# Optimization experiments

Measured on AMD Instinct MI355X. Metric: run time of the kernel, lower is better.

The kernel has to match this reference:

```python
import jax, jax.numpy as jnp
import numpy as np

N_EMBD = 1024
N_HEAD = 16
LATENT = 64
HEAD_DIM = N_EMBD // N_HEAD
B, T = 2, 2048
SCALE = 1.0 / np.sqrt(LATENT)


def setup_inputs() -> dict:
    key = jax.random.key(0)
    ks = jax.random.split(key, 10)
    s = lambda fan_in: 1.0 / np.sqrt(fan_in)
    return {
        "x": jax.random.normal(ks[0], (B, T, N_EMBD), dtype=jnp.float32),
        "Wq": jax.random.normal(ks[1], (N_EMBD, N_EMBD), dtype=jnp.float32) * s(N_EMBD),
        "bq": jnp.zeros((N_EMBD,), dtype=jnp.float32),
        "Wk": jax.random.normal(ks[2], (N_EMBD, N_HEAD * LATENT), dtype=jnp.float32) * s(N_EMBD),
        "bk": jnp.zeros((N_HEAD * LATENT,), dtype=jnp.float32),
        "Wv": jax.random.normal(ks[3], (N_EMBD, N_HEAD * LATENT), dtype=jnp.float32) * s(N_EMBD),
        "bv": jnp.zeros((N_HEAD * LATENT,), dtype=jnp.float32),
        "Wo": jax.random.normal(ks[4], (N_HEAD * LATENT, N_EMBD), dtype=jnp.float32) * s(N_HEAD * LATENT),
        "bo": jnp.zeros((N_EMBD,), dtype=jnp.float32),
        "Wc": jax.random.normal(ks[5], (HEAD_DIM, LATENT), dtype=jnp.float32) * s(HEAD_DIM),
    }


def reference(x, Wq, bq, Wk, bk, Wv, bv, Wo, bo, Wc):
    Bv, Tv, C = x.shape
    # projections
    q = (x @ Wq + bq).reshape(Bv, Tv, N_HEAD, HEAD_DIM)        # [B,T,H,Dh]
    k = (x @ Wk + bk).reshape(Bv, Tv, N_HEAD, LATENT)          # [B,T,H,L]
    v = (x @ Wv + bv).reshape(Bv, Tv, N_HEAD, LATENT)          # [B,T,H,L]
    # compress q into latent dim: [B,T,H,L]
    qc = jnp.einsum("bthd,dl->bthl", q, Wc)
    # attention scores [B,H,T,T]
    att = jnp.einsum("bthl,bshl->bhts", qc, k) * SCALE
    causal = jnp.tril(jnp.ones((Tv, Tv), dtype=bool))
    att = jnp.where(causal[None, None], att, -jnp.inf)
    att = jax.nn.softmax(att, axis=-1)
    y = jnp.einsum("bhts,bshl->bthl", att, v).reshape(Bv, Tv, N_HEAD * LATENT)
    return y @ Wo + bo
```

## Files before the change

### kernel.cpp

```cpp
#include <hip/hip_runtime.h>
#include <stdint.h>

#define TT 2048
#define BB 2
#define MROWS (BB*TT)
#define LSCALE 0.18033688011112043f

typedef unsigned short u16;
typedef __bf16 bf16x8 __attribute__((ext_vector_type(8)));
typedef float f32x4 __attribute__((ext_vector_type(4)));
typedef short s16x8 __attribute__((ext_vector_type(8)));
typedef unsigned short u16x4 __attribute__((ext_vector_type(4)));

#define GLOBAL_AS const __attribute__((address_space(1))) void*
#define LDS_AS __attribute__((address_space(3))) void*

__device__ __forceinline__ u16 f2b(float f){
  uint32_t u = __builtin_bit_cast(uint32_t, f);
  u = (u + 0x7FFFu + ((u >> 16) & 1u)) >> 16;
  return (u16)u;
}

__global__ void cvt_bf16(const float* __restrict__ in, u16* __restrict__ out, int n4){
  int i = blockIdx.x * 256 + threadIdx.x;
  if (i < n4){
    float4 v = ((const float4*)in)[i];
    u16x4 o; o.x = f2b(v.x); o.y = f2b(v.y); o.z = f2b(v.z); o.w = f2b(v.w);
    ((u16x4*)out)[i] = o;
  }
}

__global__ __launch_bounds__(256) void build_wqc(const float* __restrict__ Wq,
                                                 const float* __restrict__ Wc,
                                                 float* __restrict__ Wqc){
  __shared__ float wc[4096];
  const int t = threadIdx.x;
  #pragma unroll
  for (int i = 0; i < 16; ++i) wc[i * 256 + t] = Wc[i * 256 + t];
  __syncthreads();
  const int idx = blockIdx.x * 256 + t;
  const int d = idx >> 6;
  const int h = (idx >> 2) & 15;
  const int lq = idx & 3;
  float wqr[64];
  const float4* wq4 = (const float4*)(Wq + (size_t)d * 1024 + h * 64);
  #pragma unroll
  for (int i = 0; i < 16; ++i){
    float4 v = wq4[i];
    wqr[i * 4 + 0] = v.x; wqr[i * 4 + 1] = v.y; wqr[i * 4 + 2] = v.z; wqr[i * 4 + 3] = v.w;
  }
  float* outp = Wqc + (size_t)d * 1024 + h * 64 + lq * 16;
  #pragma unroll
  for (int j = 0; j < 16; ++j){
    int lc = lq * 16 + j;
    float acc = 0.f;
    #pragma unroll
    for (int dd = 0; dd < 64; ++dd) acc += wqr[dd] * wc[dd * 64 + lc];
    outp[j] = acc;
  }
}

__global__ void build_bqc(const float* __restrict__ bq, const float* __restrict__ Wc,
                          float* __restrict__ bqc){
  int n = blockIdx.x * 256 + threadIdx.x;
  int h = n >> 6, lc = n & 63;
  float acc = 0.f;
  for (int dd = 0; dd < 64; ++dd) acc += bq[h * 64 + dd] * Wc[dd * 64 + lc];
  bqc[n] = acc;
}

__global__ void transpose_w4(const float* __restrict__ s0, const float* __restrict__ s1,
                             const float* __restrict__ s2, const float* __restrict__ s3,
                             u16* __restrict__ o0, u16* __restrict__ o1,
                             u16* __restrict__ o2, u16* __restrict__ o3){
  const int z = blockIdx.z;
  const float* in = (z == 0) ? s0 : (z == 1) ? s1 : (z == 2) ? s2 : s3;
  u16* out = (z == 0) ? o0 : (z == 1) ? o1 : (z == 2) ? o2 : o3;
  __shared__ float t[32][33];
  int tx = threadIdx.x & 31, ty = threadIdx.x >> 5;
  int c0 = blockIdx.x * 32, r0 = blockIdx.y * 32;
  #pragma unroll
  for (int i = 0; i < 32; i += 8)
    t[ty + i][tx] = in[(size_t)(r0 + ty + i) * 1024 + c0 + tx];
  __syncthreads();
  #pragma unroll
  for (int i = 0; i < 32; i += 8)
    out[(size_t)(c0 + ty + i) * 1024 + r0 + tx] = f2b(t[tx][ty + i]);
}

__global__ void transpose_v(const u16* __restrict__ vb, u16* __restrict__ vt){
  __shared__ u16 t[32][34];
  int tx = threadIdx.x & 31, ty = threadIdx.x >> 5;
  int s0 = blockIdx.x * 32, d0 = blockIdx.y * 32, bh = blockIdx.z;
  int b = bh >> 4, h = bh & 15;
  #pragma unroll
  for (int i = 0; i < 32; i += 8)
    t[ty + i][tx] = vb[(size_t)(b * TT + s0 + ty + i) * 1024 + h * 64 + d0 + tx];
  __syncthreads();
  #pragma unroll
  for (int i = 0; i < 32; i += 8)
    vt[((size_t)bh * 64 + d0 + ty + i) * TT + s0 + tx] = t[tx][ty + i];
}

__device__ __forceinline__ void gemm_tile(const u16* __restrict__ A, const u16* __restrict__ BT,
                                          int m0, int n0, int K, f32x4 (&acc)[4][4],
                                          u16* As, u16* Bs, int tid){
  const int wv = tid >> 6, l = tid & 63;
  const int aoff = ((wv >> 1) * 64 + (l & 15)) * 32 + ((l >> 4) << 3);
  const int boff = ((wv & 1) * 64 + (l & 15)) * 32 + ((l >> 4) << 3);
  const int ob0 = wv * 1024 + l * 16;
  for (int kt = 0; kt < K; kt += 32){
    __syncthreads();
    #pragma unroll
    for (int j = 0; j < 2; ++j){
      int ob = ob0 + j * 4096;
      int row = ob >> 6, col = (ob & 63) >> 1;
      __builtin_amdgcn_global_load_lds((GLOBAL_AS)(A + (size_t)(m0 + row) * 1024 + kt + col),
                                       (LDS_AS)(As + wv * 512 + j * 2048), 16, 0, 0);
      __builtin_amdgcn_global_load_lds((GLOBAL_AS)(BT + (size_t)(n0 + row) * 1024 + kt + col),
                                       (LDS_AS)(Bs + wv * 512 + j * 2048), 16, 0, 0);
    }
    __syncthreads();
    bf16x8 av[4], bw[4];
    #pragma unroll
    for (int m = 0; m < 4; ++m) av[m] = *(const bf16x8*)(As + aoff + m * 512);
    #pragma unroll
    for (int n = 0; n < 4; ++n) bw[n] = *(const bf16x8*)(Bs + boff + n * 512);
    #pragma unroll
    for (int m = 0; m < 4; ++m)
      #pragma unroll
      for (int n = 0; n < 4; ++n)
        acc[m][n] = __builtin_amdgcn_mfma_f32_16x16x32_bf16(av[m], bw[n], acc[m][n], 0, 0, 0);
  }
}

__global__ __launch_bounds__(256) void gemm_qkv(
    const u16* __restrict__ xb,
    const u16* __restrict__ W0T, const u16* __restrict__ W1T, const u16* __restrict__ W2T,
    const float* __restrict__ b0, const float* __restrict__ b1, const float* __restrict__ b2,
    u16* __restrict__ o0, u16* __restrict__ o1, u16* __restrict__ o2){
  __shared__ u16 As[4096], Bs[4096];
  const int z = blockIdx.z;
  const u16* BT = (z == 0) ? W0T : (z == 1) ? W1T : W2T;
  const float* bias = (z == 0) ? b0 : (z == 1) ? b1 : b2;
  u16* Out = (z == 0) ? o0 : (z == 1) ? o1 : o2;
  const float osc = (z == 0) ? LSCALE : 1.0f;
  const int n0 = blockIdx.x * 128, m0 = blockIdx.y * 128;
  const int tid = threadIdx.x, wv = tid >> 6, l = tid & 63;
  f32x4 acc[4][4] = {};
  gemm_tile(xb, BT, m0, n0, 1024, acc, As, Bs, tid);
  const int wr = wv >> 1, wc = wv & 1;
  #pragma unroll
  for (int n = 0; n < 4; ++n){
    int col = n0 + wc * 64 + n * 16 + (l & 15);
    float bb = bias[col];
    #pragma unroll
    for (int m = 0; m < 4; ++m){
      int r0 = m0 + wr * 64 + m * 16 + ((l >> 4) << 2);
      #pragma unroll
      for (int r = 0; r < 4; ++r)
        Out[(size_t)(r0 + r) * 1024 + col] = f2b((acc[m][n][r] + bb) * osc);
    }
  }
}

__global__ __launch_bounds__(256) void gemm_fp32out(
    const u16* __restrict__ A, const u16* __restrict__ BT,
    const float* __restrict__ bias, float* __restrict__ Out){
  __shared__ u16 As[4096], Bs[4096];
  const int n0 = blockIdx.x * 128, m0 = blockIdx.y * 128;
  const int tid = threadIdx.x, wv = tid >> 6, l = tid & 63;
  f32x4 acc[4][4] = {};
  gemm_tile(A, BT, m0, n0, 1024, acc, As, Bs, tid);
  const int wr = wv >> 1, wc = wv & 1;
  #pragma unroll
  for (int n = 0; n < 4; ++n){
    int col = n0 + wc * 64 + n * 16 + (l & 15);
    float bb = bias[col];
    #pragma unroll
    for (int m = 0; m < 4; ++m){
      int r0 = m0 + wr * 64 + m * 16 + ((l >> 4) << 2);
      #pragma unroll
      for (int r = 0; r < 4; ++r)
        Out[(size_t)(r0 + r) * 1024 + col] = acc[m][n][r] + bb;
    }
  }
}

__global__ __launch_bounds__(256) void attn(
    const u16* __restrict__ qcg, const u16* __restrict__ kg,
    const u16* __restrict__ vtg, u16* __restrict__ yg){
  __shared__ u16 Ks[2][4096], Vs[2][4096];
  __shared__ u16 Ps[4 * 16 * 64];
  const int idx = blockIdx.x;
  const int qt = 31 - (idx >> 5), bh = idx & 31;
  const int b = bh >> 4, h = bh & 15;
  const int q0 = qt * 64;
  const int tid = threadIdx.x, wv = tid >> 6, l = tid & 63;
  const int c4 = l >> 4, q16 = l & 15;
  const size_t base = (size_t)b * TT * 1024 + h * 64;
  const u16* Q = qcg + base;
  const u16* K = kg + base;
  const u16* Vt = vtg + (size_t)bh * 64 * TT;

  const int sr = tid >> 3;
  const int sc = (tid & 7) ^ (sr & 7);
  const u16* gK = K + (size_t)sr * 1024 + sc * 8;
  const u16* gV = Vt + (size_t)sr * TT + sc * 8;

  __builtin_amdgcn_global_load_lds((GLOBAL_AS)gK, (LDS_AS)(&Ks[0][0] + wv * 512), 16, 0, 0);
  __builtin_amdgcn_global_load_lds((GLOBAL_AS)(gK + 32 * 1024), (LDS_AS)(&Ks[0][0] + 2048 + wv * 512), 16, 0, 0);
  __builtin_amdgcn_global_load_lds((GLOBAL_AS)gV, (LDS_AS)(&Vs[0][0] + wv * 512), 16, 0, 0);
  __builtin_amdgcn_global_load_lds((GLOBAL_AS)(gV + 32 * TT), (LDS_AS)(&Vs[0][0] + 2048 + wv * 512), 16, 0, 0);

  bf16x8 qf[2];
  {
    int qr = q0 + wv * 16 + q16;
    #pragma unroll
    for (int ks = 0; ks < 2; ++ks)
      qf[ks] = *(const bf16x8*)(Q + (size_t)qr * 1024 + ks * 32 + (c4 << 3));
  }
  f32x4 yacc[4] = {};
  float mrow = -1e30f, srow = 0.f;

  uint32_t* const PsW = (uint32_t*)Ps + wv * 512 + q16 * 32;
  const int pm = (q16 & 7) << 2;

  const int nt = qt + 1;
  for (int st = 0; st < nt; ++st){
    const int cur = st & 1;
    const u16* Kc = &Ks[cur][0];
    const u16* Vc = &Vs[cur][0];
    if (st + 1 < nt){
      const int s1 = (st + 1) * 64;
      u16* kd = &Ks[cur ^ 1][0] + wv * 512;
      u16* vd = &Vs[cur ^ 1][0] + wv * 512;
      __builtin_amdgcn_global_load_lds((GLOBAL_AS)(gK + (size_t)s1 * 1024), (LDS_AS)kd, 16, 0, 0);
      __builtin_amdgcn_global_load_lds((GLOBAL_AS)(gK + (size_t)(s1 + 32) * 1024), (LDS_AS)(kd + 2048), 16, 0, 0);
      __builtin_amdgcn_global_load_lds((GLOBAL_AS)(gV + s1), (LDS_AS)vd, 16, 0, 0);
      __builtin_amdgcn_global_load_lds((GLOBAL_AS)(gV + s1 + 32 * TT), (LDS_AS)(vd + 2048), 16, 0, 0);
      asm volatile("s_waitcnt vmcnt(4)" ::: "memory");
    } else {
      asm volatile("s_waitcnt vmcnt(0)" ::: "memory");
    }
    __builtin_amdgcn_sched_barrier(0);
    __builtin_amdgcn_s_barrier();
    __builtin_amdgcn_sched_barrier(0);
    const int s0 = st * 64;
    f32x4 sf[4] = {};
    __builtin_amdgcn_s_setprio(1);
    #pragma unroll
    for (int ks = 0; ks < 2; ++ks)
      #pragma unroll
      for (int nf = 0; nf < 4; ++nf){
        int r = nf * 16 + q16, c = ks * 4 + c4;
        bf16x8 kf = *(const bf16x8*)(Kc + (r * 8 + (c ^ (r & 7))) * 8);
        sf[nf] = __builtin_amdgcn_mfma_f32_16x16x32_bf16(kf, qf[ks], sf[nf], 0, 0, 0);
      }
    __builtin_amdgcn_s_setprio(0);
    const int qa = q0 + wv * 16 + q16;
    float p[4][4];
    const bool domask = (st == nt - 1);
    #pragma unroll
    for (int nf = 0; nf < 4; ++nf)
      #pragma unroll
      for (int r = 0; r < 4; ++r){
        float v_ = sf[nf][r];
        if (domask && (s0 + nf * 16 + c4 * 4 + r > qa)) v_ = -1e30f;
        p[nf][r] = v_;
      }
    float tmax = p[0][0];
    #pragma unroll
    for (int nf = 0; nf < 4; ++nf)
      #pragma unroll
      for (int r = 0; r < 4; ++r) tmax = fmaxf(tmax, p[nf][r]);
    tmax = fmaxf(tmax, __shfl_xor(tmax, 16));
    tmax = fmaxf(tmax, __shfl_xor(tmax, 32));
    if (__any(tmax > mrow + 8.0f)){
      float mnew = fmaxf(mrow, tmax);
      float resc = exp2f(mrow - mnew);
      srow *= resc;
      mrow = mnew;
      float rq[4];
      #pragma unroll
      for (int r = 0; r < 4; ++r) rq[r] = __shfl(resc, (l & 48) | (c4 * 4 + r));
      #pragma unroll
      for (int df = 0; df < 4; ++df)
        #pragma unroll
        for (int r = 0; r < 4; ++r) yacc[df][r] *= rq[r];
    }
    float tsum = 0.f;
    #pragma unroll
    for (int nf = 0; nf < 4; ++nf)
      #pragma unroll
      for (int r = 0; r < 4; ++r){ float e = exp2f(p[nf][r] - mrow); p[nf][r] = e; tsum += e; }
    tsum += __shfl_xor(tsum, 16);
    tsum += __shfl_xor(tsum, 32);
    srow += tsum;
    #pragma unroll
    for (int nf = 0; nf < 4; ++nf){
      uint32_t w0, w1;
      asm volatile("v_cvt_pk_bf16_f32 %0, %1, %2" : "=v"(w0) : "v"(p[nf][0]), "v"(p[nf][1]));
      asm volatile("v_cvt_pk_bf16_f32 %0, %1, %2" : "=v"(w1) : "v"(p[nf][2]), "v"(p[nf][3]));
      *(uint64_t*)(PsW + ((nf * 8 + c4 * 2) ^ pm)) = (uint64_t)w0 | ((uint64_t)w1 << 32);
    }
    asm volatile("s_waitcnt lgkmcnt(0)" ::: "memory");
    __builtin_amdgcn_sched_barrier(0);
    __builtin_amdgcn_s_setprio(1);
    #pragma unroll
    for (int ks2 = 0; ks2 < 2; ++ks2){
      bf16x8 pf = *(const bf16x8*)(PsW + ((ks2 * 16 + c4 * 4) ^ pm));
      #pragma unroll
      for (int df = 0; df < 4; ++df){
        int rd = df * 16 + q16, cd = ks2 * 4 + c4;
        bf16x8 vf = *(const bf16x8*)(Vc + (rd * 8 + (cd ^ (rd & 7))) * 8);
        yacc[df] = __builtin_amdgcn_mfma_f32_16x16x32_bf16(pf, vf, yacc[df], 0, 0, 0);
      }
    }
    __builtin_amdgcn_s_setprio(0);
    __builtin_amdgcn_s_barrier();
  }
  float sq[4];
  #pragma unroll
  for (int r = 0; r < 4; ++r) sq[r] = __shfl(srow, (l & 48) | (c4 * 4 + r));
  #pragma unroll
  for (int df = 0; df < 4; ++df){
    int d = df * 16 + q16;
    int qq = q0 + wv * 16 + c4 * 4;
    #pragma unroll
    for (int r = 0; r < 4; ++r){
      float val = yacc[df][r] / sq[r];
      yg[(size_t)(b * TT + qq + r) * 1024 + h * 64 + d] = f2b(val);
    }
  }
}

extern "C" void kernel_launch(void* const* d_in, const int* in_sizes, int n_in,
                              void* d_out, int out_size, void* d_ws, size_t ws_size,
                              hipStream_t stream){
  (void)in_sizes; (void)n_in; (void)out_size; (void)ws_size;
  const float* x  = (const float*)d_in[0];
  const float* Wq = (const float*)d_in[1];
  const float* bq = (const float*)d_in[2];
  const float* Wk = (const float*)d_in[3];
  const float* bk = (const float*)d_in[4];
  const float* Wv = (const float*)d_in[5];
  const float* bv = (const float*)d_in[6];
  const float* Wo = (const float*)d_in[7];
  const float* bo = (const float*)d_in[8];
  const float* Wc = (const float*)d_in[9];
  float* out = (float*)d_out;

  char* wsb = (char*)d_ws;
  u16* xb    = (u16*)(wsb);
  u16* yb    = (u16*)(wsb);
  u16* qcb   = (u16*)(wsb + (8u  << 20));
  u16* kb    = (u16*)(wsb + (16u << 20));
  u16* vb    = (u16*)(wsb + (24u << 20));
  u16* vtb   = (u16*)(wsb + (32u << 20));
  u16* WqcT  = (u16*)(wsb + (40u << 20));
  u16* WkT   = (u16*)(wsb + (42u << 20));
  u16* WvT   = (u16*)(wsb + (44u << 20));
  u16* WoT   = (u16*)(wsb + (46u << 20));
  float* bqc  = (float*)(wsb + (48u << 20));
  float* Wqcf = (float*)(wsb + (48u << 20) + 8192);

  cvt_bf16<<<4096, 256, 0, stream>>>(x, xb, MROWS * 1024 / 4);
  build_wqc<<<256, 256, 0, stream>>>(Wq, Wc, Wqcf);
  build_bqc<<<4, 256, 0, stream>>>(bq, Wc, bqc);
  transpose_w4<<<dim3(32, 32, 4), 256, 0, stream>>>(Wqcf, Wk, Wv, Wo, WqcT, WkT, WvT, WoT);
  gemm_qkv<<<dim3(8, 32, 3), 256, 0, stream>>>(xb, WqcT, WkT, WvT, bqc, bk, bv, qcb, kb, vb);
  transpose_v<<<dim3(64, 2, 32), 256, 0, stream>>>(vb, vtb);
  attn<<<dim3(1024), 256, 0, stream>>>(qcb, kb, vtb, yb);
  gemm_fp32out<<<dim3(8, 32), 256, 0, stream>>>(yb, WoT, bo, out);
}
```

Measured before the change: 131.4 us.

## Split long causal attention rows across two blocks and merge with combine kernel

Query tiles 15-31 now have their key range split in half across two blocks, each writing unnormalized partial outputs plus row max and sum. A new combine kernel merges the two halves with log-sum-exp weights. This is meant to balance the causal workload and raise occupancy. The K/V staging moves from async global-to-LDS double buffering to register-prefetched single-buffer LDS stores, which frees LDS for a higher occupancy target. The build_bqc kernel is also folded into build_wqc to drop a launch. Costs are an extra kernel launch, extra partial-output traffic, and bf16 rounding of the partial outputs.

```diff
diff --git a/kernel.cpp b/kernel.cpp
--- a/kernel.cpp
+++ b/kernel.cpp
@@ -11,6 +11,7 @@
 typedef float f32x4 __attribute__((ext_vector_type(4)));
 typedef short s16x8 __attribute__((ext_vector_type(8)));
 typedef unsigned short u16x4 __attribute__((ext_vector_type(4)));
+typedef int i32x4 __attribute__((ext_vector_type(4)));
 
 #define GLOBAL_AS const __attribute__((address_space(1))) void*
 #define LDS_AS __attribute__((address_space(3))) void*
@@ -19,6 +20,9 @@
   uint32_t u = __builtin_bit_cast(uint32_t, f);
   u = (u + 0x7FFFu + ((u >> 16) & 1u)) >> 16;
   return (u16)u;
+}
+__device__ __forceinline__ float b2f(u16 u){
+  return __builtin_bit_cast(float, (uint32_t)u << 16);
 }
 
 __global__ void cvt_bf16(const float* __restrict__ in, u16* __restrict__ out, int n4){
@@ -32,12 +36,26 @@
 
 __global__ __launch_bounds__(256) void build_wqc(const float* __restrict__ Wq,
                                                  const float* __restrict__ Wc,
-                                                 float* __restrict__ Wqc){
+                                                 const float* __restrict__ bq,
+                                                 float* __restrict__ Wqc,
+                                                 float* __restrict__ bqc){
   __shared__ float wc[4096];
   const int t = threadIdx.x;
   #pragma unroll
   for (int i = 0; i < 16; ++i) wc[i * 256 + t] = Wc[i * 256 + t];
   __syncthreads();
+  if (blockIdx.x == 256){
+    #pragma unroll
+    for (int i = 0; i < 4; ++i){
+      int nn = t * 4 + i;
+      int h = nn >> 6, lc = nn & 63;
+      float acc = 0.f;
+      #pragma unroll
+      for (int dd = 0; dd < 64; ++dd) acc += bq[h * 64 + dd] * wc[dd * 64 + lc];
+      bqc[nn] = acc;
+    }
+    return;
+  }
   const int idx = blockIdx.x * 256 + t;
   const int d = idx >> 6;
   const int h = (idx >> 2) & 15;
@@ -58,15 +76,6 @@
     for (int dd = 0; dd < 64; ++dd) acc += wqr[dd] * wc[dd * 64 + lc];
     outp[j] = acc;
   }
-}
-
-__global__ void build_bqc(const float* __restrict__ bq, const float* __restrict__ Wc,
-                          float* __restrict__ bqc){
-  int n = blockIdx.x * 256 + threadIdx.x;
-  int h = n >> 6, lc = n & 63;
-  float acc = 0.f;
-  for (int dd = 0; dd < 64; ++dd) acc += bq[h * 64 + dd] * Wc[dd * 64 + lc];
-  bqc[n] = acc;
 }
 
 __global__ void transpose_w4(const float* __restrict__ s0, const float* __restrict__ s1,
@@ -187,13 +196,28 @@
   }
 }
 
-__global__ __launch_bounds__(256) void attn(
+#define NSPLIT 1088
+__global__ __launch_bounds__(256, 6) void attn(
     const u16* __restrict__ qcg, const u16* __restrict__ kg,
-    const u16* __restrict__ vtg, u16* __restrict__ yg){
-  __shared__ u16 Ks[2][4096], Vs[2][4096];
-  __shared__ u16 Ps[4 * 16 * 64];
+    const u16* __restrict__ vtg, u16* __restrict__ yg,
+    u16* __restrict__ yp, float* __restrict__ mp, float* __restrict__ lp){
+  __shared__ u16 Ks[4096], Vs[4096];
+  __shared__ u16 Ps[4096];
   const int idx = blockIdx.x;
-  const int qt = 31 - (idx >> 5), bh = idx & 31;
+  int qt, bh, st0, st1, pid;
+  if (idx < NSPLIT){
+    qt = 31 - (idx >> 6);
+    int sub = idx & 63; bh = sub >> 1;
+    int ntf = qt + 1, hh = (ntf + 1) >> 1;
+    st0 = (sub & 1) ? hh : 0;
+    st1 = (sub & 1) ? ntf : hh;
+    pid = idx;
+  } else {
+    int i2 = idx - NSPLIT;
+    qt = 14 - (i2 >> 5); bh = i2 & 31;
+    st0 = 0; st1 = qt + 1;
+    pid = -1;
+  }
   const int b = bh >> 4, h = bh & 15;
   const int q0 = qt * 64;
   const int tid = threadIdx.x, wv = tid >> 6, l = tid & 63;
@@ -208,10 +232,14 @@
   const u16* gK = K + (size_t)sr * 1024 + sc * 8;
   const u16* gV = Vt + (size_t)sr * TT + sc * 8;
 
-  __builtin_amdgcn_global_load_lds((GLOBAL_AS)gK, (LDS_AS)(&Ks[0][0] + wv * 512), 16, 0, 0);
-  __builtin_amdgcn_global_load_lds((GLOBAL_AS)(gK + 32 * 1024), (LDS_AS)(&Ks[0][0] + 2048 + wv * 512), 16, 0, 0);
-  __builtin_amdgcn_global_load_lds((GLOBAL_AS)gV, (LDS_AS)(&Vs[0][0] + wv * 512), 16, 0, 0);
-  __builtin_amdgcn_global_load_lds((GLOBAL_AS)(gV + 32 * TT), (LDS_AS)(&Vs[0][0] + 2048 + wv * 512), 16, 0, 0);
+  i32x4 kp0, kp1, vp0, vp1;
+  {
+    const size_t o = (size_t)st0 * 64;
+    kp0 = *(const i32x4*)(gK + o * 1024);
+    kp1 = *(const i32x4*)(gK + (o + 32) * 1024);
+    vp0 = *(const i32x4*)(gV + o);
+    vp1 = *(const i32x4*)(gV + o + 32 * TT);
+  }
 
   bf16x8 qf[2];
   {
@@ -226,23 +254,24 @@
   uint32_t* const PsW = (uint32_t*)Ps + wv * 512 + q16 * 32;
   const int pm = (q16 & 7) << 2;
 
-  const int nt = qt + 1;
-  for (int st = 0; st < nt; ++st){
-    const int cur = st & 1;
-    const u16* Kc = &Ks[cur][0];
-    const u16* Vc = &Vs[cur][0];
-    if (st + 1 < nt){
-      const int s1 = (st + 1) * 64;
-      u16* kd = &Ks[cur ^ 1][0] + wv * 512;
-      u16* vd = &Vs[cur ^ 1][0] + wv * 512;
-      __builtin_amdgcn_global_load_lds((GLOBAL_AS)(gK + (size_t)s1 * 1024), (LDS_AS)kd, 16, 0, 0);
-      __builtin_amdgcn_global_load_lds((GLOBAL_AS)(gK + (size_t)(s1 + 32) * 1024), (LDS_AS)(kd + 2048), 16, 0, 0);
-      __builtin_amdgcn_global_load_lds((GLOBAL_AS)(gV + s1), (LDS_AS)vd, 16, 0, 0);
-      __builtin_amdgcn_global_load_lds((GLOBAL_AS)(gV + s1 + 32 * TT), (LDS_AS)(vd + 2048), 16, 0, 0);
-      asm volatile("s_waitcnt vmcnt(4)" ::: "memory");
-    } else {
-      asm volatile("s_waitcnt vmcnt(0)" ::: "memory");
-    }
+  for (int st = st0; st < st1; ++st){
+    if (st != st0){
+      __builtin_amdgcn_sched_barrier(0);
+      __builtin_amdgcn_s_barrier();
+      __builtin_amdgcn_sched_barrier(0);
+    }
+    ((i32x4*)Ks)[tid]       = kp0;
+    ((i32x4*)Ks)[256 + tid] = kp1;
+    ((i32x4*)Vs)[tid]       = vp0;
+    ((i32x4*)Vs)[256 + tid] = vp1;
+    if (st + 1 < st1){
+      const size_t o = (size_t)(st + 1) * 64;
+      kp0 = *(const i32x4*)(gK + o * 1024);
+      kp1 = *(const i32x4*)(gK + (o + 32) * 1024);
+      vp0 = *(const i32x4*)(gV + o);
+      vp1 = *(const i32x4*)(gV + o + 32 * TT);
+    }
+    asm volatile("s_waitcnt lgkmcnt(0)" ::: "memory");
     __builtin_amdgcn_sched_barrier(0);
     __builtin_amdgcn_s_barrier();
     __builtin_amdgcn_sched_barrier(0);
@@ -254,13 +283,13 @@
       #pragma unroll
       for (int nf = 0; nf < 4; ++nf){
         int r = nf * 16 + q16, c = ks * 4 + c4;
-        bf16x8 kf = *(const bf16x8*)(Kc + (r * 8 + (c ^ (r & 7))) * 8);
+        bf16x8 kf = *(const bf16x8*)(Ks + (r * 8 + (c ^ (r & 7))) * 8);
         sf[nf] = __builtin_amdgcn_mfma_f32_16x16x32_bf16(kf, qf[ks], sf[nf], 0, 0, 0);
       }
     __builtin_amdgcn_s_setprio(0);
     const int qa = q0 + wv * 16 + q16;
     float p[4][4];
-    const bool domask = (st == nt - 1);
+    const bool domask = (st == qt);
     #pragma unroll
     for (int nf = 0; nf < 4; ++nf)
       #pragma unroll
@@ -313,25 +342,69 @@
       #pragma unroll
       for (int df = 0; df < 4; ++df){
         int rd = df * 16 + q16, cd = ks2 * 4 + c4;
-        bf16x8 vf = *(const bf16x8*)(Vc + (rd * 8 + (cd ^ (rd & 7))) * 8);
+        bf16x8 vf = *(const bf16x8*)(Vs + (rd * 8 + (cd ^ (rd & 7))) * 8);
         yacc[df] = __builtin_amdgcn_mfma_f32_16x16x32_bf16(pf, vf, yacc[df], 0, 0, 0);
       }
     }
     __builtin_amdgcn_s_setprio(0);
-    __builtin_amdgcn_s_barrier();
-  }
-  float sq[4];
-  #pragma unroll
-  for (int r = 0; r < 4; ++r) sq[r] = __shfl(srow, (l & 48) | (c4 * 4 + r));
-  #pragma unroll
-  for (int df = 0; df < 4; ++df){
-    int d = df * 16 + q16;
-    int qq = q0 + wv * 16 + c4 * 4;
-    #pragma unroll
-    for (int r = 0; r < 4; ++r){
-      float val = yacc[df][r] / sq[r];
-      yg[(size_t)(b * TT + qq + r) * 1024 + h * 64 + d] = f2b(val);
-    }
+  }
+
+  if (pid >= 0){
+    #pragma unroll
+    for (int df = 0; df < 4; ++df){
+      int d = df * 16 + q16;
+      int qq = wv * 16 + c4 * 4;
+      #pragma unroll
+      for (int r = 0; r < 4; ++r)
+        yp[(size_t)pid * 4096 + (qq + r) * 64 + d] = f2b(yacc[df][r]);
+    }
+    if (c4 == 0){
+      mp[pid * 64 + wv * 16 + q16] = mrow;
+      lp[pid * 64 + wv * 16 + q16] = srow;
+    }
+  } else {
+    float sq[4];
+    #pragma unroll
+    for (int r = 0; r < 4; ++r) sq[r] = __shfl(srow, (l & 48) | (c4 * 4 + r));
+    #pragma unroll
+    for (int df = 0; df < 4; ++df){
+      int d = df * 16 + q16;
+      int qq = q0 + wv * 16 + c4 * 4;
+      #pragma unroll
+      for (int r = 0; r < 4; ++r){
+        float val = yacc[df][r] / sq[r];
+        yg[(size_t)(b * TT + qq + r) * 1024 + h * 64 + d] = f2b(val);
+      }
+    }
+  }
+}
+
+__global__ __launch_bounds__(256) void attn_combine(
+    const u16* __restrict__ yp, const float* __restrict__ mp, const float* __restrict__ lp,
+    u16* __restrict__ yg){
+  const int blk = blockIdx.x;
+  const int qt = 15 + (blk >> 5), bh = blk & 31;
+  const int pid0 = (31 - qt) * 64 + bh * 2;
+  const int t = threadIdx.x;
+  const int q = t >> 2, dc = (t & 3) * 16;
+  float m1 = mp[pid0 * 64 + q], m2 = mp[(pid0 + 1) * 64 + q];
+  float l1 = lp[pid0 * 64 + q], l2 = lp[(pid0 + 1) * 64 + q];
+  float ms = fmaxf(m1, m2);
+  float w1 = exp2f(m1 - ms), w2 = exp2f(m2 - ms);
+  float inv = 1.f / (l1 * w1 + l2 * w2);
+  w1 *= inv; w2 *= inv;
+  const int b = bh >> 4, h = bh & 15;
+  const s16x8* p1 = (const s16x8*)(yp + (size_t)pid0 * 4096 + q * 64 + dc);
+  const s16x8* p2 = (const s16x8*)(yp + (size_t)(pid0 + 1) * 4096 + q * 64 + dc);
+  u16* dst = yg + (size_t)(b * TT + qt * 64 + q) * 1024 + h * 64 + dc;
+  #pragma unroll
+  for (int j2 = 0; j2 < 2; ++j2){
+    s16x8 a = p1[j2], c = p2[j2];
+    s16x8 o;
+    #pragma unroll
+    for (int j = 0; j < 8; ++j)
+      o[j] = (short)f2b(b2f((u16)a[j]) * w1 + b2f((u16)c[j]) * w2);
+    *(s16x8*)(dst + j2 * 8) = o;
   }
 }
 
@@ -357,20 +430,23 @@
   u16* qcb   = (u16*)(wsb + (8u  << 20));
   u16* kb    = (u16*)(wsb + (16u << 20));
   u16* vb    = (u16*)(wsb + (24u << 20));
-  u16* vtb   = (u16*)(wsb + (32u << 20));
-  u16* WqcT  = (u16*)(wsb + (40u << 20));
-  u16* WkT   = (u16*)(wsb + (42u << 20));
-  u16* WvT   = (u16*)(wsb + (44u << 20));
-  u16* WoT   = (u16*)(wsb + (46u << 20));
-  float* bqc  = (float*)(wsb + (48u << 20));
-  float* Wqcf = (float*)(wsb + (48u << 20) + 8192);
+  u16* yp    = (u16*)(wsb + (24u << 20));
+  u16* vtb   = (u16*)(wsb + (33u << 20));
+  float* Wqcf = (float*)(wsb + (33u << 20));
+  float* mp  = (float*)(wsb + (41u << 20));
+  float* lp  = (float*)(wsb + (41u << 20) + (1u<<19));
+  u16* WqcT  = (u16*)(wsb + (42u << 20));
+  u16* WkT   = (u16*)(wsb + (44u << 20));
+  u16* WvT   = (u16*)(wsb + (46u << 20));
+  u16* WoT   = (u16*)(wsb + (48u << 20));
+  float* bqc  = (float*)(wsb + (50u << 20));
 
   cvt_bf16<<<4096, 256, 0, stream>>>(x, xb, MROWS * 1024 / 4);
-  build_wqc<<<256, 256, 0, stream>>>(Wq, Wc, Wqcf);
-  build_bqc<<<4, 256, 0, stream>>>(bq, Wc, bqc);
+  build_wqc<<<257, 256, 0, stream>>>(Wq, Wc, bq, Wqcf, bqc);
   transpose_w4<<<dim3(32, 32, 4), 256, 0, stream>>>(Wqcf, Wk, Wv, Wo, WqcT, WkT, WvT, WoT);
   gemm_qkv<<<dim3(8, 32, 3), 256, 0, stream>>>(xb, WqcT, WkT, WvT, bqc, bk, bv, qcb, kb, vb);
   transpose_v<<<dim3(64, 2, 32), 256, 0, stream>>>(vb, vtb);
-  attn<<<dim3(1024), 256, 0, stream>>>(qcb, kb, vtb, yb);
+  attn<<<dim3(1568), 256, 0, stream>>>(qcb, kb, vtb, yb, yp, mp, lp);
+  attn_combine<<<dim3(544), 256, 0, stream>>>(yp, mp, lp, yb);
   gemm_fp32out<<<dim3(8, 32), 256, 0, stream>>>(yb, WoT, bo, out);
 }
```

Result: slower. 161.5 us (+22.9%).

## Restructure attention into single-wave blocks loading K/V directly to registers

Applied to the files above, without the earlier changes.

The attention kernel moves from 256-thread blocks that stage K and V tiles in double-buffered LDS via global_load_lds to single-wave blocks. Each block handles 32 query rows as two 16-row sub-tiles and loads K and V fragments straight from global memory into registers, removing block-wide barriers and LDS staging. The bias-compression kernel is folded into an extra block of build_wqc to save a launch, and workspace offsets are reshuffled. The trade-off is that K/V reuse now comes only from the cache rather than LDS sharing across four waves, with more global load traffic per query row. Register pressure also rises from holding kf/vf fragments.

```diff
diff --git a/kernel.cpp b/kernel.cpp
--- a/kernel.cpp
+++ b/kernel.cpp
@@ -32,12 +32,26 @@
 
 __global__ __launch_bounds__(256) void build_wqc(const float* __restrict__ Wq,
                                                  const float* __restrict__ Wc,
-                                                 float* __restrict__ Wqc){
+                                                 const float* __restrict__ bq,
+                                                 float* __restrict__ Wqc,
+                                                 float* __restrict__ bqc){
   __shared__ float wc[4096];
   const int t = threadIdx.x;
   #pragma unroll
   for (int i = 0; i < 16; ++i) wc[i * 256 + t] = Wc[i * 256 + t];
   __syncthreads();
+  if (blockIdx.x == 256){
+    #pragma unroll
+    for (int i = 0; i < 4; ++i){
+      int nn = t * 4 + i;
+      int h = nn >> 6, lc = nn & 63;
+      float acc = 0.f;
+      #pragma unroll
+      for (int dd = 0; dd < 64; ++dd) acc += bq[h * 64 + dd] * wc[dd * 64 + lc];
+      bqc[nn] = acc;
+    }
+    return;
+  }
   const int idx = blockIdx.x * 256 + t;
   const int d = idx >> 6;
   const int h = (idx >> 2) & 15;
@@ -58,15 +72,6 @@
     for (int dd = 0; dd < 64; ++dd) acc += wqr[dd] * wc[dd * 64 + lc];
     outp[j] = acc;
   }
-}
-
-__global__ void build_bqc(const float* __restrict__ bq, const float* __restrict__ Wc,
-                          float* __restrict__ bqc){
-  int n = blockIdx.x * 256 + threadIdx.x;
-  int h = n >> 6, lc = n & 63;
-  float acc = 0.f;
-  for (int dd = 0; dd < 64; ++dd) acc += bq[h * 64 + dd] * Wc[dd * 64 + lc];
-  bqc[n] = acc;
 }
 
 __global__ void transpose_w4(const float* __restrict__ s0, const float* __restrict__ s1,
@@ -187,150 +192,136 @@
   }
 }
 
-__global__ __launch_bounds__(256) void attn(
+__global__ __launch_bounds__(64, 3) void attn(
     const u16* __restrict__ qcg, const u16* __restrict__ kg,
     const u16* __restrict__ vtg, u16* __restrict__ yg){
-  __shared__ u16 Ks[2][4096], Vs[2][4096];
-  __shared__ u16 Ps[4 * 16 * 64];
+  __shared__ u16 Ps[2][1024];
   const int idx = blockIdx.x;
-  const int qt = 31 - (idx >> 5), bh = idx & 31;
+  const int bh = idx & 31;
+  const int qg = 63 - (idx >> 5);
   const int b = bh >> 4, h = bh & 15;
-  const int q0 = qt * 64;
-  const int tid = threadIdx.x, wv = tid >> 6, l = tid & 63;
+  const int q0 = qg * 32;
+  const int l = threadIdx.x & 63;
   const int c4 = l >> 4, q16 = l & 15;
   const size_t base = (size_t)b * TT * 1024 + h * 64;
   const u16* Q = qcg + base;
   const u16* K = kg + base;
   const u16* Vt = vtg + (size_t)bh * 64 * TT;
 
-  const int sr = tid >> 3;
-  const int sc = (tid & 7) ^ (sr & 7);
-  const u16* gK = K + (size_t)sr * 1024 + sc * 8;
-  const u16* gV = Vt + (size_t)sr * TT + sc * 8;
-
-  __builtin_amdgcn_global_load_lds((GLOBAL_AS)gK, (LDS_AS)(&Ks[0][0] + wv * 512), 16, 0, 0);
-  __builtin_amdgcn_global_load_lds((GLOBAL_AS)(gK + 32 * 1024), (LDS_AS)(&Ks[0][0] + 2048 + wv * 512), 16, 0, 0);
-  __builtin_amdgcn_global_load_lds((GLOBAL_AS)gV, (LDS_AS)(&Vs[0][0] + wv * 512), 16, 0, 0);
-  __builtin_amdgcn_global_load_lds((GLOBAL_AS)(gV + 32 * TT), (LDS_AS)(&Vs[0][0] + 2048 + wv * 512), 16, 0, 0);
-
-  bf16x8 qf[2];
-  {
-    int qr = q0 + wv * 16 + q16;
+  bf16x8 qf[2][2];
+  #pragma unroll
+  for (int qs = 0; qs < 2; ++qs){
+    int qr = q0 + qs * 16 + q16;
     #pragma unroll
     for (int ks = 0; ks < 2; ++ks)
-      qf[ks] = *(const bf16x8*)(Q + (size_t)qr * 1024 + ks * 32 + (c4 << 3));
-  }
-  f32x4 yacc[4] = {};
-  float mrow = -1e30f, srow = 0.f;
-
-  uint32_t* const PsW = (uint32_t*)Ps + wv * 512 + q16 * 32;
+      qf[qs][ks] = *(const bf16x8*)(Q + (size_t)qr * 1024 + ks * 32 + c4 * 8);
+  }
+  f32x4 yacc[2][4] = {};
+  float mrow[2] = {-1e30f, -1e30f}, srow[2] = {0.f, 0.f};
+
   const int pm = (q16 & 7) << 2;
 
-  const int nt = qt + 1;
+  const int nt = (qg >> 1) + 1;
   for (int st = 0; st < nt; ++st){
-    const int cur = st & 1;
-    const u16* Kc = &Ks[cur][0];
-    const u16* Vc = &Vs[cur][0];
-    if (st + 1 < nt){
-      const int s1 = (st + 1) * 64;
-      u16* kd = &Ks[cur ^ 1][0] + wv * 512;
-      u16* vd = &Vs[cur ^ 1][0] + wv * 512;
-      __builtin_amdgcn_global_load_lds((GLOBAL_AS)(gK + (size_t)s1 * 1024), (LDS_AS)kd, 16, 0, 0);
-      __builtin_amdgcn_global_load_lds((GLOBAL_AS)(gK + (size_t)(s1 + 32) * 1024), (LDS_AS)(kd + 2048), 16, 0, 0);
-      __builtin_amdgcn_global_load_lds((GLOBAL_AS)(gV + s1), (LDS_AS)vd, 16, 0, 0);
-      __builtin_amdgcn_global_load_lds((GLOBAL_AS)(gV + s1 + 32 * TT), (LDS_AS)(vd + 2048), 16, 0, 0);
-      asm volatile("s_waitcnt vmcnt(4)" ::: "memory");
-    } else {
-      asm volatile("s_waitcnt vmcnt(0)" ::: "memory");
-    }
-    __builtin_amdgcn_sched_barrier(0);
-    __builtin_amdgcn_s_barrier();
-    __builtin_amdgcn_sched_barrier(0);
     const int s0 = st * 64;
-    f32x4 sf[4] = {};
-    __builtin_amdgcn_s_setprio(1);
+    bf16x8 kf[2][4];
     #pragma unroll
     for (int ks = 0; ks < 2; ++ks)
       #pragma unroll
+      for (int nf = 0; nf < 4; ++nf)
+        kf[ks][nf] = *(const bf16x8*)(K + (size_t)(s0 + nf * 16 + q16) * 1024 + ks * 32 + c4 * 8);
+    f32x4 sf[2][4] = {};
+    #pragma unroll
+    for (int ks = 0; ks < 2; ++ks)
+      #pragma unroll
       for (int nf = 0; nf < 4; ++nf){
-        int r = nf * 16 + q16, c = ks * 4 + c4;
-        bf16x8 kf = *(const bf16x8*)(Kc + (r * 8 + (c ^ (r & 7))) * 8);
-        sf[nf] = __builtin_amdgcn_mfma_f32_16x16x32_bf16(kf, qf[ks], sf[nf], 0, 0, 0);
-      }
-    __builtin_amdgcn_s_setprio(0);
-    const int qa = q0 + wv * 16 + q16;
-    float p[4][4];
+        sf[0][nf] = __builtin_amdgcn_mfma_f32_16x16x32_bf16(kf[ks][nf], qf[0][ks], sf[0][nf], 0, 0, 0);
+        sf[1][nf] = __builtin_amdgcn_mfma_f32_16x16x32_bf16(kf[ks][nf], qf[1][ks], sf[1][nf], 0, 0, 0);
+      }
+    bf16x8 vf[2][4];
+    #pragma unroll
+    for (int ks2 = 0; ks2 < 2; ++ks2)
+      #pragma unroll
+      for (int df = 0; df < 4; ++df)
+        vf[ks2][df] = *(const bf16x8*)(Vt + (size_t)(df * 16 + q16) * TT + s0 + ks2 * 32 + c4 * 8);
     const bool domask = (st == nt - 1);
     #pragma unroll
-    for (int nf = 0; nf < 4; ++nf)
-      #pragma unroll
-      for (int r = 0; r < 4; ++r){
-        float v_ = sf[nf][r];
-        if (domask && (s0 + nf * 16 + c4 * 4 + r > qa)) v_ = -1e30f;
-        p[nf][r] = v_;
-      }
-    float tmax = p[0][0];
-    #pragma unroll
-    for (int nf = 0; nf < 4; ++nf)
-      #pragma unroll
-      for (int r = 0; r < 4; ++r) tmax = fmaxf(tmax, p[nf][r]);
-    tmax = fmaxf(tmax, __shfl_xor(tmax, 16));
-    tmax = fmaxf(tmax, __shfl_xor(tmax, 32));
-    if (__any(tmax > mrow + 8.0f)){
-      float mnew = fmaxf(mrow, tmax);
-      float resc = exp2f(mrow - mnew);
-      srow *= resc;
-      mrow = mnew;
-      float rq[4];
-      #pragma unroll
-      for (int r = 0; r < 4; ++r) rq[r] = __shfl(resc, (l & 48) | (c4 * 4 + r));
-      #pragma unroll
-      for (int df = 0; df < 4; ++df)
-        #pragma unroll
-        for (int r = 0; r < 4; ++r) yacc[df][r] *= rq[r];
-    }
-    float tsum = 0.f;
-    #pragma unroll
-    for (int nf = 0; nf < 4; ++nf)
-      #pragma unroll
-      for (int r = 0; r < 4; ++r){ float e = exp2f(p[nf][r] - mrow); p[nf][r] = e; tsum += e; }
-    tsum += __shfl_xor(tsum, 16);
-    tsum += __shfl_xor(tsum, 32);
-    srow += tsum;
-    #pragma unroll
-    for (int nf = 0; nf < 4; ++nf){
-      uint32_t w0, w1;
-      asm volatile("v_cvt_pk_bf16_f32 %0, %1, %2" : "=v"(w0) : "v"(p[nf][0]), "v"(p[nf][1]));
-      asm volatile("v_cvt_pk_bf16_f32 %0, %1, %2" : "=v"(w1) : "v"(p[nf][2]), "v"(p[nf][3]));
-      *(uint64_t*)(PsW + ((nf * 8 + c4 * 2) ^ pm)) = (uint64_t)w0 | ((uint64_t)w1 << 32);
+    for (int qs = 0; qs < 2; ++qs){
+      const int qa = q0 + qs * 16 + q16;
+      float p[4][4];
+      #pragma unroll
+      for (int nf = 0; nf < 4; ++nf)
+        #pragma unroll
+        for (int r = 0; r < 4; ++r){
+          float v_ = sf[qs][nf][r];
+          if (domask && (s0 + nf * 16 + c4 * 4 + r > qa)) v_ = -1e30f;
+          p[nf][r] = v_;
+        }
+      float tmax = p[0][0];
+      #pragma unroll
+      for (int nf = 0; nf < 4; ++nf)
+        #pragma unroll
+        for (int r = 0; r < 4; ++r) tmax = fmaxf(tmax, p[nf][r]);
+      tmax = fmaxf(tmax, __shfl_xor(tmax, 16));
+      tmax = fmaxf(tmax, __shfl_xor(tmax, 32));
+      if (__any(tmax > mrow[qs] + 8.0f)){
+        float mnew = fmaxf(mrow[qs], tmax);
+        float resc = exp2f(mrow[qs] - mnew);
+        srow[qs] *= resc;
+        mrow[qs] = mnew;
+        float rq[4];
+        #pragma unroll
+        for (int r = 0; r < 4; ++r) rq[r] = __shfl(resc, (l & 48) | (c4 * 4 + r));
+        #pragma unroll
+        for (int df = 0; df < 4; ++df)
+          #pragma unroll
+          for (int r = 0; r < 4; ++r) yacc[qs][df][r] *= rq[r];
+      }
+      float tsum = 0.f;
+      #pragma unroll
+      for (int nf = 0; nf < 4; ++nf)
+        #pragma unroll
+        for (int r = 0; r < 4; ++r){ float e = exp2f(p[nf][r] - mrow[qs]); p[nf][r] = e; tsum += e; }
+      tsum += __shfl_xor(tsum, 16);
+      tsum += __shfl_xor(tsum, 32);
+      srow[qs] += tsum;
+      uint32_t* dst = (uint32_t*)&Ps[qs][0] + q16 * 32;
+      #pragma unroll
+      for (int nf = 0; nf < 4; ++nf){
+        uint32_t w0, w1;
+        asm volatile("v_cvt_pk_bf16_f32 %0, %1, %2" : "=v"(w0) : "v"(p[nf][0]), "v"(p[nf][1]));
+        asm volatile("v_cvt_pk_bf16_f32 %0, %1, %2" : "=v"(w1) : "v"(p[nf][2]), "v"(p[nf][3]));
+        *(uint64_t*)(dst + ((nf * 8 + c4 * 2) ^ pm)) = (uint64_t)w0 | ((uint64_t)w1 << 32);
+      }
     }
     asm volatile("s_waitcnt lgkmcnt(0)" ::: "memory");
     __builtin_amdgcn_sched_barrier(0);
-    __builtin_amdgcn_s_setprio(1);
-    #pragma unroll
-    for (int ks2 = 0; ks2 < 2; ++ks2){
-      bf16x8 pf = *(const bf16x8*)(PsW + ((ks2 * 16 + c4 * 4) ^ pm));
-      #pragma unroll
-      for (int df = 0; df < 4; ++df){
-        int rd = df * 16 + q16, cd = ks2 * 4 + c4;
-        bf16x8 vf = *(const bf16x8*)(Vc + (rd * 8 + (cd ^ (rd & 7))) * 8);
-        yacc[df] = __builtin_amdgcn_mfma_f32_16x16x32_bf16(pf, vf, yacc[df], 0, 0, 0);
-      }
-    }
-    __builtin_amdgcn_s_setprio(0);
-    __builtin_amdgcn_s_barrier();
-  }
-  float sq[4];
-  #pragma unroll
-  for (int r = 0; r < 4; ++r) sq[r] = __shfl(srow, (l & 48) | (c4 * 4 + r));
-  #pragma unroll
-  for (int df = 0; df < 4; ++df){
-    int d = df * 16 + q16;
-    int qq = q0 + wv * 16 + c4 * 4;
-    #pragma unroll
-    for (int r = 0; r < 4; ++r){
-      float val = yacc[df][r] / sq[r];
-      yg[(size_t)(b * TT + qq + r) * 1024 + h * 64 + d] = f2b(val);
+    #pragma unroll
+    for (int qs = 0; qs < 2; ++qs){
+      const uint32_t* src = (const uint32_t*)&Ps[qs][0] + q16 * 32;
+      #pragma unroll
+      for (int ks2 = 0; ks2 < 2; ++ks2){
+        bf16x8 pf = *(const bf16x8*)(src + ((ks2 * 16 + c4 * 4) ^ pm));
+        #pragma unroll
+        for (int df = 0; df < 4; ++df)
+          yacc[qs][df] = __builtin_amdgcn_mfma_f32_16x16x32_bf16(pf, vf[ks2][df], yacc[qs][df], 0, 0, 0);
+      }
+    }
+  }
+  #pragma unroll
+  for (int qs = 0; qs < 2; ++qs){
+    float sq[4];
+    #pragma unroll
+    for (int r = 0; r < 4; ++r) sq[r] = __shfl(srow[qs], (l & 48) | (c4 * 4 + r));
+    #pragma unroll
+    for (int df = 0; df < 4; ++df){
+      int d = df * 16 + q16;
+      int qq = q0 + qs * 16 + c4 * 4;
+      #pragma unroll
+      for (int r = 0; r < 4; ++r){
+        float val = yacc[qs][df][r] / sq[r];
+        yg[(size_t)(b * TT + qq + r) * 1024 + h * 64 + d] = f2b(val);
+      }
     }
   }
 }
@@ -357,20 +348,19 @@
   u16* qcb   = (u16*)(wsb + (8u  << 20));
   u16* kb    = (u16*)(wsb + (16u << 20));
   u16* vb    = (u16*)(wsb + (24u << 20));
-  u16* vtb   = (u16*)(wsb + (32u << 20));
-  u16* WqcT  = (u16*)(wsb + (40u << 20));
-  u16* WkT   = (u16*)(wsb + (42u << 20));
-  u16* WvT   = (u16*)(wsb + (44u << 20));
-  u16* WoT   = (u16*)(wsb + (46u << 20));
-  float* bqc  = (float*)(wsb + (48u << 20));
-  float* Wqcf = (float*)(wsb + (48u << 20) + 8192);
+  u16* vtb   = (u16*)(wsb + (33u << 20));
+  float* Wqcf = (float*)(wsb + (33u << 20));
+  u16* WqcT  = (u16*)(wsb + (42u << 20));
+  u16* WkT   = (u16*)(wsb + (44u << 20));
+  u16* WvT   = (u16*)(wsb + (46u << 20));
+  u16* WoT   = (u16*)(wsb + (48u << 20));
+  float* bqc  = (float*)(wsb + (50u << 20));
 
   cvt_bf16<<<4096, 256, 0, stream>>>(x, xb, MROWS * 1024 / 4);
-  build_wqc<<<256, 256, 0, stream>>>(Wq, Wc, Wqcf);
-  build_bqc<<<4, 256, 0, stream>>>(bq, Wc, bqc);
+  build_wqc<<<257, 256, 0, stream>>>(Wq, Wc, bq, Wqcf, bqc);
   transpose_w4<<<dim3(32, 32, 4), 256, 0, stream>>>(Wqcf, Wk, Wv, Wo, WqcT, WkT, WvT, WoT);
   gemm_qkv<<<dim3(8, 32, 3), 256, 0, stream>>>(xb, WqcT, WkT, WvT, bqc, bk, bv, qcb, kb, vb);
   transpose_v<<<dim3(64, 2, 32), 256, 0, stream>>>(vb, vtb);
-  attn<<<dim3(1024), 256, 0, stream>>>(qcb, kb, vtb, yb);
+  attn<<<dim3(2048), 64, 0, stream>>>(qcb, kb, vtb, yb);
   gemm_fp32out<<<dim3(8, 32), 256, 0, stream>>>(yb, WoT, bo, out);
 }
```

Result: slower. 157.0 us (+19.4%).
